# Optimization experiments

Measured on AMD Instinct MI355X. Metric: run time of the kernel, lower is better.

## Reference

```python
import jax, jax.numpy as jnp
import numpy as np

B, C, H, G, NCLS = 32, 256, 128, 128, 2  # graphs, nodes-per-graph==in_channels, hidden, matrix pool, classes
N = B * C                                # total nodes = 8192
E = 131072


def setup_inputs() -> dict:
    key = jax.random.key(0)
    ks = jax.random.split(key, 12)
    gain = 5.0 / 3.0
    xav = gain * np.sqrt(6.0 / (C + C))  # xavier_uniform bound for [C,C]
    return {
        "x": jax.random.normal(ks[0], (N, C), jnp.float32),
        "edge_index": jax.random.randint(ks[1], (2, E), 0, N),
        "graph_id": jax.random.randint(ks[2], (B,), 0, G),
        "batch": jnp.arange(N) // C,
        "pert_W": jax.random.uniform(ks[3], (G, C, C), jnp.float32, -xav, xav),
        "pert_b": jax.random.uniform(ks[4], (G, C, C), jnp.float32, -xav, xav),
        "mask_W": jax.random.uniform(ks[5], (G, C, C), jnp.float32, -xav, xav),
        "gcn_w0": jax.random.normal(ks[6], (C, H), jnp.float32) / np.sqrt(C),
        "gcn_w1": jax.random.normal(ks[7], (H, H), jnp.float32) / np.sqrt(H),
        "gcn_w2": jax.random.normal(ks[8], (H, H), jnp.float32) / np.sqrt(H),
        "mlp_W": jax.random.normal(ks[9], (2 * H, NCLS), jnp.float32) / np.sqrt(2 * H),
        "mlp_b": jnp.zeros((NCLS,), jnp.float32),
    }


def _hard_where(s):
    # MyWhere: 0 if s <= 0.5 else 1
    return jnp.where(s <= 0.5, 0.0, 1.0).astype(s.dtype)


def _predictor(x, adj, batch, gcn_w0, gcn_w1, gcn_w2, mlp_W, mlp_b):
    # GCN encoder: h <- relu(A @ h @ W); readout = concat(mean-pool, max-pool); MLP+sigmoid
    h = x
    for W in (gcn_w0, gcn_w1, gcn_w2):
        h = jax.nn.relu(adj @ (h @ W))
    sums = jax.ops.segment_sum(h, batch, num_segments=B)
    cnt = jax.ops.segment_sum(jnp.ones((h.shape[0], 1), h.dtype), batch, num_segments=B)
    mean = sums / jnp.maximum(cnt, 1.0)
    mx = jax.ops.segment_max(h, batch, num_segments=B)
    pooled = jnp.concatenate([mean, mx], axis=-1)  # [B, 2H]
    return jax.nn.sigmoid(pooled @ mlp_W + mlp_b)


def reference(x, edge_index, graph_id, batch, pert_W, pert_b, mask_W,
              gcn_w0, gcn_w1, gcn_w2, mlp_W, mlp_b):
    # dense adjacency (duplicate edges sum, matching sparse_coo.to_dense)
    adj = jnp.zeros((N, N), jnp.float32).at[edge_index[0], edge_index[1]].add(1.0)
    P = pert_W[graph_id]    # [B, C, C] block-diag blocks
    bias = pert_b[graph_id]  # [B, C, C] block-diag bias blocks
    # block_diag(P) @ adj == per-block GEMM over row stripes
    PA = jnp.einsum('bij,bjn->bin', P, adj.reshape(B, C, N))  # [B, C, N]
    PA = PA.reshape(B, C, B, C).at[jnp.arange(B), :, jnp.arange(B), :].add(bias)
    PA = PA.reshape(N, N)
    pert_adj = _hard_where(jax.nn.sigmoid(PA))
    M = _hard_where(jax.nn.sigmoid(mask_W[graph_id].reshape(N, C)))
    x_masked = M * x
    pred = _predictor(x, adj, batch, gcn_w0, gcn_w1, gcn_w2, mlp_W, mlp_b)
    aug_pred = _predictor(x_masked, pert_adj, batch, gcn_w0, gcn_w1, gcn_w2, mlp_W, mlp_b)
    return (adj, pert_adj, M, pred, aug_pred, x_masked)
```

## Files before the change

### kernel.cpp

```cpp
#include <hip/hip_runtime.h>
#include <hip/hip_bf16.h>

#define NN 8192
#define CC 256
#define BBg 32
#define HH 128
#define EE 131072

typedef __attribute__((ext_vector_type(8))) short short8;
typedef __attribute__((ext_vector_type(4))) float f32x4;
typedef unsigned long long ull;

__device__ __forceinline__ float hard01(float v) {
    if (v >= 1e-6f) return 1.0f;
    if (v <= 0.0f) return 0.0f;
    float ef = (float)exp(-(double)v);
    float s = 1.0f / (1.0f + ef);
    return (s > 0.5f) ? 1.0f : 0.0f;
}

__device__ __forceinline__ unsigned short f2bf(float f) {
    unsigned u = __float_as_uint(f);
    u += 0x7FFFu + ((u >> 16) & 1u);
    return (unsigned short)(u >> 16);
}
__device__ __forceinline__ float bf2f(unsigned short b) {
    return __uint_as_float(((unsigned)b) << 16);
}

__global__ void k_hist_mask(const int* __restrict__ ei, int* __restrict__ rowcnt,
                            int* __restrict__ colcnt, unsigned char* __restrict__ coljs,
                            const float* __restrict__ maskW, const int* __restrict__ gid,
                            const float* __restrict__ x, float* __restrict__ Mo,
                            float* __restrict__ xm) {
    int blk = blockIdx.x, t = threadIdx.x;
    if (blk < 512) {
        int e = blk * 256 + t;
        int r = ei[e], c = ei[EE + e];
        atomicAdd(&rowcnt[r], 1);
        int idx = (r >> 8) * NN + c;
        int slot = atomicAdd(&colcnt[idx], 1);
        if (slot < 16) coljs[(size_t)idx * 16 + slot] = (unsigned char)(r & 255);
    } else {
        int i = (blk - 512) * 256 + t;
        int base = i * 4;
        int r = base >> 8;
        int c = base & 255;
        int g = gid[r >> 8];
        float4 mv = *(const float4*)(maskW + ((size_t)g << 16) + ((size_t)(r & 255) << 8) + c);
        float4 xv = *(const float4*)(x + ((size_t)r << 8) + c);
        float4 m, o;
        m.x = hard01(mv.x); m.y = hard01(mv.y); m.z = hard01(mv.z); m.w = hard01(mv.w);
        o.x = m.x * xv.x; o.y = m.y * xv.y; o.z = m.z * xv.z; o.w = m.w * xv.w;
        *(float4*)(Mo + ((size_t)r << 8) + c) = m;
        *(float4*)(xm + ((size_t)r << 8) + c) = o;
    }
}

__global__ void __launch_bounds__(256) k_scan_pertadj(
        const int* __restrict__ rowcnt, int* __restrict__ rowptr,
        int* __restrict__ rowfill,
        const float* __restrict__ pertW, const float* __restrict__ pertB,
        const int* __restrict__ gid, const int* __restrict__ colcnt,
        const unsigned char* __restrict__ coljs,
        float* __restrict__ padj, unsigned char* __restrict__ padjbits) {
    __shared__ float Pl[32][257];
    __shared__ int sums[256];
    int t = threadIdx.x;
    if (blockIdx.x == 0) {
        int base = t * 32;
        int loc[32];
        int s = 0;
        #pragma unroll
        for (int i = 0; i < 32; ++i) { loc[i] = s; s += rowcnt[base + i]; }
        sums[t] = s;
        __syncthreads();
        if (t == 0) {
            int a = 0;
            for (int i = 0; i < 256; ++i) { int v = sums[i]; sums[i] = a; a += v; }
            rowptr[NN] = a;
        }
        __syncthreads();
        int off = sums[t];
        #pragma unroll
        for (int i = 0; i < 32; ++i) {
            rowptr[base + i] = off + loc[i];
            rowfill[base + i] = off + loc[i];
        }
        return;
    }
    int bid = blockIdx.x - 1;
    int nc = bid & 3, rt = (bid >> 2) & 7, b = bid >> 5;
    int g = gid[b];
    const float* src = pertW + ((size_t)g << 16) + (size_t)rt * 32 * CC;
    #pragma unroll 4
    for (int i = 0; i < 32; ++i) Pl[i][t] = src[i * CC + t];
    __syncthreads();
    int ty = t >> 6, tx = t & 63;
    int ro = ty * 8;
    const float* bsrc = pertB + ((size_t)g << 16) + (size_t)(rt * 32 + ro) * CC;
    for (int it = 0; it < 4; ++it) {
        int n0 = nc * 2048 + it * 512 + tx * 8;
        float s[8][8];
        #pragma unroll
        for (int ii = 0; ii < 8; ++ii)
            #pragma unroll
            for (int cc = 0; cc < 8; ++cc) s[ii][cc] = 0.0f;
        #pragma unroll
        for (int half = 0; half < 2; ++half) {
            int n = n0 + half * 4;
            int cidx = b * NN + n;
            int4 cnt4 = *(const int4*)(colcnt + cidx);
            const uint4* jp = (const uint4*)(coljs + (size_t)cidx * 16);
            #pragma unroll
            for (int cc = 0; cc < 4; ++cc) {
                int cnt = (&cnt4.x)[cc];
                cnt = cnt > 16 ? 16 : cnt;
                if (cnt == 0) continue;
                uint4 jv = jp[cc];
                for (int q = 0; q < cnt; ++q) {
                    unsigned word = (q < 8) ? ((q < 4) ? jv.x : jv.y)
                                            : ((q < 12) ? jv.z : jv.w);
                    int j = (word >> ((q & 3) * 8)) & 255;
                    #pragma unroll
                    for (int ii = 0; ii < 8; ++ii) s[ii][half * 4 + cc] += Pl[ro + ii][j];
                }
            }
        }
        bool diag = ((n0 >> 8) == b);
        #pragma unroll
        for (int ii = 0; ii < 8; ++ii) {
            if (diag) {
                const float* bp = bsrc + (size_t)ii * CC + (n0 & 255);
                #pragma unroll
                for (int cc = 0; cc < 8; ++cc) s[ii][cc] += bp[cc];
            }
            float f[8];
            unsigned byte = 0;
            #pragma unroll
            for (int cc = 0; cc < 8; ++cc) {
                f[cc] = hard01(s[ii][cc]);
                if (f[cc] != 0.f) byte |= (1u << cc);
            }
            size_t ob = (size_t)(b * CC + rt * 32 + ro + ii) * NN + n0;
            float4 f0, f1;
            f0.x = f[0]; f0.y = f[1]; f0.z = f[2]; f0.w = f[3];
            f1.x = f[4]; f1.y = f[5]; f1.z = f[6]; f1.w = f[7];
            *(float4*)(padj + ob) = f0;
            *(float4*)(padj + ob + 4) = f1;
            size_t bb = (size_t)(b * CC + rt * 32 + ro + ii) * (NN / 8)
                        + nc * 256 + it * 64 + tx;
            padjbits[bb] = (unsigned char)byte;
        }
    }
}

__device__ __forceinline__ void gemm_dual_body(
        int mt, int t,
        const float* __restrict__ Ap, const float* __restrict__ Aa,
        const float* __restrict__ W, float* __restrict__ Zp,
        unsigned short* __restrict__ Zthi, unsigned short* __restrict__ Ztlo,
        int K, int relu, int aparts, int apstride,
        float (*Alp)[68], float (*Ala)[68], float (*Wl)[132]) {
    int ty = t >> 3, tx = t & 7;
    float accp[16], acca[16];
    #pragma unroll
    for (int u = 0; u < 16; ++u) { accp[u] = 0.0f; acca[u] = 0.0f; }
    for (int kc = 0; kc < K; kc += 64) {
        int row = t >> 3, q = t & 7;
        {
            const float* ap = Ap + (size_t)(mt * 32 + row) * K + kc + q * 8;
            float4 f0 = *(const float4*)ap;
            float4 f1 = *(const float4*)(ap + 4);
            if (relu) {
                f0.x = fmaxf(f0.x, 0.f); f0.y = fmaxf(f0.y, 0.f);
                f0.z = fmaxf(f0.z, 0.f); f0.w = fmaxf(f0.w, 0.f);
                f1.x = fmaxf(f1.x, 0.f); f1.y = fmaxf(f1.y, 0.f);
                f1.z = fmaxf(f1.z, 0.f); f1.w = fmaxf(f1.w, 0.f);
            }
            *(float4*)&Alp[row][q * 8] = f0;
            *(float4*)&Alp[row][q * 8 + 4] = f1;
        }
        {
            const float* ap = Aa + (size_t)(mt * 32 + row) * K + kc + q * 8;
            float4 f0 = *(const float4*)ap;
            float4 f1 = *(const float4*)(ap + 4);
            for (int p = 1; p < aparts; ++p) {
                float4 g0 = *(const float4*)(ap + (size_t)p * apstride);
                float4 g1 = *(const float4*)(ap + (size_t)p * apstride + 4);
                f0.x += g0.x; f0.y += g0.y; f0.z += g0.z; f0.w += g0.w;
                f1.x += g1.x; f1.y += g1.y; f1.z += g1.z; f1.w += g1.w;
            }
            if (relu) {
                f0.x = fmaxf(f0.x, 0.f); f0.y = fmaxf(f0.y, 0.f);
                f0.z = fmaxf(f0.z, 0.f); f0.w = fmaxf(f0.w, 0.f);
                f1.x = fmaxf(f1.x, 0.f); f1.y = fmaxf(f1.y, 0.f);
                f1.z = fmaxf(f1.z, 0.f); f1.w = fmaxf(f1.w, 0.f);
            }
            *(float4*)&Ala[row][q * 8] = f0;
            *(float4*)&Ala[row][q * 8 + 4] = f1;
        }
        {
            int wrow = t >> 2, wq = t & 3;
            const float* wp = W + (size_t)(kc + wrow) * HH + wq * 32;
            #pragma unroll
            for (int u = 0; u < 32; u += 4)
                *(float4*)&Wl[wrow][wq * 32 + u] = *(const float4*)(wp + u);
        }
        __syncthreads();
        #pragma unroll 2
        for (int kk = 0; kk < 64; ++kk) {
            float a = Alp[ty][kk];
            float b2 = Ala[ty][kk];
            #pragma unroll
            for (int u = 0; u < 16; u += 4) {
                float4 wv = *(const float4*)(&Wl[kk][tx * 16 + u]);
                accp[u + 0] += a * wv.x; accp[u + 1] += a * wv.y;
                accp[u + 2] += a * wv.z; accp[u + 3] += a * wv.w;
                acca[u + 0] += b2 * wv.x; acca[u + 1] += b2 * wv.y;
                acca[u + 2] += b2 * wv.z; acca[u + 3] += b2 * wv.w;
            }
        }
        __syncthreads();
    }
    {
        float* cp = Zp + (size_t)(mt * 32 + ty) * HH + tx * 16;
        #pragma unroll
        for (int u = 0; u < 16; u += 4) {
            float4 f;
            f.x = accp[u]; f.y = accp[u + 1]; f.z = accp[u + 2]; f.w = accp[u + 3];
            *(float4*)(cp + u) = f;
        }
    }
    {
        __syncthreads();
        float* Tl = &Wl[0][0];
        #pragma unroll
        for (int u = 0; u < 16; ++u) Tl[ty * 132 + tx * 16 + u] = acca[u];
        __syncthreads();
        int col = t >> 1, half = t & 1;
        unsigned short hu[16] __attribute__((aligned(16)));
        unsigned short lu[16] __attribute__((aligned(16)));
        #pragma unroll
        for (int rr = 0; rr < 16; ++rr) {
            float v = Tl[(half * 16 + rr) * 132 + col];
            unsigned short hb = f2bf(v);
            hu[rr] = hb;
            lu[rr] = f2bf(v - bf2f(hb));
        }
        size_t ob = (size_t)col * NN + mt * 32 + half * 16;
        *(uint4*)(Zthi + ob)     = *(const uint4*)&hu[0];
        *(uint4*)(Zthi + ob + 8) = *(const uint4*)&hu[8];
        *(uint4*)(Ztlo + ob)     = *(const uint4*)&lu[0];
        *(uint4*)(Ztlo + ob + 8) = *(const uint4*)&lu[8];
    }
}

__global__ void __launch_bounds__(256) k_gemm_fill(
        const float* __restrict__ Ap, const float* __restrict__ Aa,
        const float* __restrict__ W, float* __restrict__ Zp,
        unsigned short* __restrict__ Zthi, unsigned short* __restrict__ Ztlo,
        int K, int relu, int aparts, int apstride,
        const int* __restrict__ ei, int* __restrict__ rowfill,
        int* __restrict__ csrcol) {
    __shared__ float Alp[32][68];
    __shared__ float Ala[32][68];
    __shared__ float Wl[64][132];
    int blk = blockIdx.x, t = threadIdx.x;
    if (blk < 256) {
        gemm_dual_body(blk, t, Ap, Aa, W, Zp, Zthi, Ztlo, K, relu, aparts, apstride,
                       Alp, Ala, Wl);
    } else {
        int e = (blk - 256) * 256 + t;
        int r = ei[e], c = ei[EE + e];
        int pos = atomicAdd(&rowfill[r], 1);
        csrcol[pos] = c;
    }
}

__global__ void __launch_bounds__(256) k_gemm_dual(
        const float* __restrict__ Ap, const float* __restrict__ Aa,
        const float* __restrict__ W, float* __restrict__ Zp,
        unsigned short* __restrict__ Zthi, unsigned short* __restrict__ Ztlo,
        int K, int relu, int aparts, int apstride) {
    __shared__ float Alp[32][68];
    __shared__ float Ala[32][68];
    __shared__ float Wl[64][132];
    gemm_dual_body(blockIdx.x, threadIdx.x, Ap, Aa, W, Zp, Zthi, Ztlo,
                   K, relu, aparts, apstride, Alp, Ala, Wl);
}

__device__ __forceinline__ void mfma_body(
        int blk, int t,
        const unsigned char* __restrict__ padjbits,
        const unsigned short* __restrict__ Zthi,
        const unsigned short* __restrict__ Ztlo,
        float* __restrict__ Sp, unsigned short* BhBase, unsigned short* BlBase) {
    int mt = blk & 31;
    int ncol = (blk >> 5) & 1;
    int sk = blk >> 6;
    int w = t >> 6, lane = t & 63;
    int quad = lane >> 4, l15 = lane & 15;
    f32x4 acc[4][4];
    #pragma unroll
    for (int m = 0; m < 4; ++m)
        #pragma unroll
        for (int i = 0; i < 4; ++i) acc[m][i] = (f32x4){0.f, 0.f, 0.f, 0.f};
    int bn = t >> 2, sub = t & 3;
    int bq = sub & 1, hilo = sub >> 1;
    const unsigned short* zsrc = (hilo ? Ztlo : Zthi)
        + (size_t)(ncol * 64 + bn) * NN + sk * 1024 + bq * 16;
    unsigned short* wb = hilo ? BlBase : BhBase;
    int row0 = mt * 256 + w * 64 + l15;
    const unsigned* ab[4];
    #pragma unroll
    for (int m = 0; m < 4; ++m)
        ab[m] = (const unsigned*)(padjbits + (size_t)(row0 + m * 16) * (NN / 8)) + sk * 32;
    int ldsw = bn * 40 + bq * 16;
    int bmb = l15 * 40 + quad * 8;
    uint4 rv0, rv1;
    unsigned bits[4], nbits[4];
    rv0 = *(const uint4*)(zsrc + 0);
    rv1 = *(const uint4*)(zsrc + 8);
    #pragma unroll
    for (int m = 0; m < 4; ++m) bits[m] = ab[m][0];
    *(uint4*)(wb + ldsw + 0) = rv0;
    *(uint4*)(wb + ldsw + 8) = rv1;
    __syncthreads();
    for (int st = 0; st < 32; ++st) {
        int cur = st & 1;
        if (st < 31) {
            int k = (st + 1) * 32;
            rv0 = *(const uint4*)(zsrc + k);
            rv1 = *(const uint4*)(zsrc + k + 8);
            #pragma unroll
            for (int m = 0; m < 4; ++m) nbits[m] = ab[m][st + 1];
        }
        short8 a[4];
        #pragma unroll
        for (int m = 0; m < 4; ++m) {
            unsigned byte = (bits[m] >> (quad * 8)) & 0xFFu;
            #pragma unroll
            for (int j = 0; j < 8; ++j)
                a[m][j] = (byte & (1u << j)) ? (short)0x3F80 : (short)0;
        }
        const unsigned short* Bh = BhBase + cur * 2560;
        const unsigned short* Bl = BlBase + cur * 2560;
        #pragma unroll
        for (int nt = 0; nt < 4; ++nt) {
            short8 fh = *(const short8*)(Bh + nt * 16 * 40 + bmb);
            short8 fl = *(const short8*)(Bl + nt * 16 * 40 + bmb);
            #pragma unroll
            for (int m = 0; m < 4; ++m) {
                acc[m][nt] = __builtin_amdgcn_mfma_f32_16x16x32_bf16(a[m], fh, acc[m][nt], 0, 0, 0);
                acc[m][nt] = __builtin_amdgcn_mfma_f32_16x16x32_bf16(a[m], fl, acc[m][nt], 0, 0, 0);
            }
        }
        if (st < 31) {
            unsigned short* wn = wb + (1 - cur) * 2560;
            *(uint4*)(wn + ldsw + 0) = rv0;
            *(uint4*)(wn + ldsw + 8) = rv1;
            #pragma unroll
            for (int m = 0; m < 4; ++m) bits[m] = nbits[m];
        }
        __syncthreads();
    }
    int dc = l15, dr = quad * 4;
    float* base = Sp + (size_t)sk * NN * HH
                + (size_t)(mt * 256 + w * 64 + dr) * HH + ncol * 64;
    #pragma unroll
    for (int m = 0; m < 4; ++m)
        #pragma unroll
        for (int nt = 0; nt < 4; ++nt)
            #pragma unroll
            for (int r = 0; r < 4; ++r)
                base[(size_t)(m * 16 + r) * HH + nt * 16 + dc] = acc[m][nt][r];
}

__device__ __forceinline__ void adj_body(
        int row, int t, unsigned* cnt,
        const int* __restrict__ rowptr, const int* __restrict__ csrcol,
        float* __restrict__ adj) {
    uint4 z = {0u, 0u, 0u, 0u};
    #pragma unroll
    for (int i = 0; i < 4; ++i) *(uint4*)&cnt[(i * 256 + t) * 4] = z;
    __syncthreads();
    int start = rowptr[row], end = rowptr[row + 1];
    for (int e = start + t; e < end; e += 256) {
        int c = csrcol[e];
        atomicAdd(&cnt[c >> 1], 1u << ((c & 1) * 16));
    }
    __syncthreads();
    float* dst = adj + (size_t)row * NN;
    #pragma unroll
    for (int i = 0; i < 8; ++i) {
        int p = i * 1024 + t * 4;
        unsigned w0 = cnt[p >> 1], w1 = cnt[(p >> 1) + 1];
        float4 f;
        f.x = (float)(w0 & 0xFFFFu); f.y = (float)(w0 >> 16);
        f.z = (float)(w1 & 0xFFFFu); f.w = (float)(w1 >> 16);
        *(float4*)(dst + p) = f;
    }
}

__device__ __forceinline__ void spmm_body(
        int bp, int t,
        const int* __restrict__ rowptr, const int* __restrict__ csrcol,
        const float* __restrict__ Z, float* __restrict__ S) {
    int row = bp * 2 + (t >> 7);
    int col = t & 127;
    int start = rowptr[row], end = rowptr[row + 1];
    float s0 = 0.f, s1 = 0.f;
    int e = start;
    for (; e + 2 <= end; e += 2) {
        int c0 = csrcol[e], c1 = csrcol[e + 1];
        s0 += Z[(size_t)c0 * HH + col];
        s1 += Z[(size_t)c1 * HH + col];
    }
    if (e < end) s0 += Z[(size_t)csrcol[e] * HH + col];
    S[(size_t)row * HH + col] = s0 + s1;
}

#define MFB 1024
#define SPB (NN / 2)

__global__ void __launch_bounds__(256, 4) k_mfma_adj_spmm(
        const unsigned char* __restrict__ padjbits,
        const unsigned short* __restrict__ Zthi,
        const unsigned short* __restrict__ Ztlo,
        float* __restrict__ Sp,
        const int* __restrict__ rowptr, const int* __restrict__ csrcol,
        float* __restrict__ adj,
        const float* __restrict__ Z, float* __restrict__ S) {
    __shared__ __align__(16) char smem[20480];
    int blk = blockIdx.x, t = threadIdx.x;
    if (blk < MFB) {
        mfma_body(blk, t, padjbits, Zthi, Ztlo, Sp,
                  (unsigned short*)smem, (unsigned short*)(smem + 10240));
    } else if (blk < MFB + SPB) {
        spmm_body(blk - MFB, t, rowptr, csrcol, Z, S);
    } else {
        adj_body(blk - (MFB + SPB), t, (unsigned*)smem, rowptr, csrcol, adj);
    }
}

__global__ void __launch_bounds__(256, 4) k_mfma_spmm2(
        const unsigned char* __restrict__ padjbits,
        const unsigned short* __restrict__ Zthi,
        const unsigned short* __restrict__ Ztlo,
        float* __restrict__ Sp,
        const int* __restrict__ rowptr, const int* __restrict__ csrcol,
        const float* __restrict__ Z, float* __restrict__ S) {
    __shared__ __align__(16) char smem[20480];
    int blk = blockIdx.x, t = threadIdx.x;
    if (blk < MFB) {
        mfma_body(blk, t, padjbits, Zthi, Ztlo, Sp,
                  (unsigned short*)smem, (unsigned short*)(smem + 10240));
    } else {
        spmm_body(blk - MFB, t, rowptr, csrcol, Z, S);
    }
}

__global__ void __launch_bounds__(256) k_pool2(const float* __restrict__ S,
                                               const float* __restrict__ Sp,
                                               const float* __restrict__ mlpW,
                                               const float* __restrict__ mlpb,
                                               float* __restrict__ pred,
                                               float* __restrict__ augp,
                                               int apstride) {
    __shared__ float ps[256], pm[256], pl[256], r0[256], r1[256];
    int aug = blockIdx.x >> 5, g = blockIdx.x & 31, t = threadIdx.x;
    const float* Sb = aug ? Sp : S;
    int parts = aug ? 8 : 1;
    float* outp = aug ? augp : pred;
    int col = t & 127, half = t >> 7;
    const float* base = Sb + (size_t)(g * CC + half * 128) * HH + col;
    float sum = 0.f, mx = -3.0e38f;
    for (int rr = 0; rr < 128; ++rr) {
        float v = base[(size_t)rr * HH];
        for (int p = 1; p < parts; ++p) v += base[(size_t)p * apstride + (size_t)rr * HH];
        v = fmaxf(v, 0.f);
        sum += v;
        mx = fmaxf(mx, v);
    }
    ps[t] = sum; pm[t] = mx;
    __syncthreads();
    if (half == 0) {
        pl[col] = (ps[col] + ps[col + 128]) * (1.0f / 256.0f);
        pl[col + 128] = fmaxf(pm[col], pm[col + 128]);
    }
    __syncthreads();
    r0[t] = pl[t] * mlpW[t * 2 + 0];
    r1[t] = pl[t] * mlpW[t * 2 + 1];
    __syncthreads();
    for (int sft = 128; sft > 0; sft >>= 1) {
        if (t < sft) { r0[t] += r0[t + sft]; r1[t] += r1[t + sft]; }
        __syncthreads();
    }
    if (t == 0) {
        float l0 = r0[0] + mlpb[0];
        float l1 = r1[0] + mlpb[1];
        outp[g * 2 + 0] = 1.0f / (1.0f + expf(-l0));
        outp[g * 2 + 1] = 1.0f / (1.0f + expf(-l1));
    }
}

extern "C" void kernel_launch(void* const* d_in, const int* in_sizes, int n_in,
                              void* d_out, int out_size, void* d_ws, size_t ws_size,
                              hipStream_t stream) {
    (void)in_sizes; (void)n_in; (void)out_size; (void)ws_size;
    const float* x     = (const float*)d_in[0];
    const int*   ei    = (const int*)d_in[1];
    const int*   gid   = (const int*)d_in[2];
    const float* pertW = (const float*)d_in[4];
    const float* pertB = (const float*)d_in[5];
    const float* maskW = (const float*)d_in[6];
    const float* w0    = (const float*)d_in[7];
    const float* w1    = (const float*)d_in[8];
    const float* w2    = (const float*)d_in[9];
    const float* mlpW  = (const float*)d_in[10];
    const float* mlpb  = (const float*)d_in[11];

    float* out  = (float*)d_out;
    float* adj  = out;
    float* padj = out + (size_t)NN * NN;
    float* Mo   = out + 2 * (size_t)NN * NN;
    float* pred = Mo + (size_t)NN * CC;
    float* augp = pred + (size_t)BBg * 2;
    float* xm   = augp + (size_t)BBg * 2;

    char* ws = (char*)d_ws;
    int*            colcnt   = (int*)ws;
    int*            rowcnt   = (int*)(ws + (1 << 20));
    int*            rowptr   = (int*)(ws + (1 << 20) + (64 << 10));
    int*            rowfill  = (int*)(ws + (1 << 20) + (128 << 10));
    unsigned char*  coljs    = (unsigned char*)(ws + (2 << 20));
    int*            csrcol   = (int*)(ws + (6 << 20));
    float*          Z        = (float*)(ws + (7 << 20));
    float*          S        = (float*)(ws + (11 << 20));
    unsigned short* Zthi     = (unsigned short*)(ws + (15 << 20));
    unsigned short* Ztlo     = (unsigned short*)(ws + (17 << 20));
    float*          Sp       = (float*)(ws + (19 << 20));
    unsigned char*  padjbits = (unsigned char*)(ws + (51 << 20));
    const int PS = NN * HH;

    hipMemsetAsync(colcnt, 0, (1 << 20) + (32 << 10), stream);
    k_hist_mask<<<2560, 256, 0, stream>>>(ei, rowcnt, colcnt, coljs,
                                          maskW, gid, x, Mo, xm);
    k_scan_pertadj<<<1025, 256, 0, stream>>>(rowcnt, rowptr, rowfill,
                                             pertW, pertB, gid, colcnt, coljs,
                                             padj, padjbits);
    k_gemm_fill<<<768, 256, 0, stream>>>(x, xm, w0, Z, Zthi, Ztlo, 256, 0, 1, 0,
                                         ei, rowfill, csrcol);
    k_mfma_adj_spmm<<<MFB + SPB + NN, 256, 0, stream>>>(
        padjbits, Zthi, Ztlo, Sp, rowptr, csrcol, adj, Z, S);
    k_gemm_dual<<<256, 256, 0, stream>>>(S, Sp, w1, Z, Zthi, Ztlo, 128, 1, 8, PS);
    k_mfma_spmm2<<<MFB + SPB, 256, 0, stream>>>(
        padjbits, Zthi, Ztlo, Sp, rowptr, csrcol, Z, S);
    k_gemm_dual<<<256, 256, 0, stream>>>(S, Sp, w2, Z, Zthi, Ztlo, 128, 1, 8, PS);
    k_mfma_spmm2<<<MFB + SPB, 256, 0, stream>>>(
        padjbits, Zthi, Ztlo, Sp, rowptr, csrcol, Z, S);
    k_pool2<<<64, 256, 0, stream>>>(S, Sp, mlpW, mlpb, pred, augp, PS);
}
```

Baseline: 1.112 ms.

## Split fused MFMA/SpMM/adj kernels and remap MFMA block indexing

```diff
diff --git a/kernel.cpp b/kernel.cpp
--- a/kernel.cpp
+++ b/kernel.cpp
@@ -296,9 +296,9 @@
         const unsigned short* __restrict__ Zthi,
         const unsigned short* __restrict__ Ztlo,
         float* __restrict__ Sp, unsigned short* BhBase, unsigned short* BlBase) {
-    int mt = blk & 31;
-    int ncol = (blk >> 5) & 1;
-    int sk = blk >> 6;
+    int sk = blk & 7;
+    int ncol = (blk >> 3) & 1;
+    int mt = blk >> 4;
     int w = t >> 6, lane = t & 63;
     int quad = lane >> 4, l15 = lane & 15;
     f32x4 acc[4][4];
@@ -373,41 +373,62 @@
         #pragma unroll
         for (int nt = 0; nt < 4; ++nt)
             #pragma unroll
-            for (int r = 0; r < 4; ++r)
-                base[(size_t)(m * 16 + r) * HH + nt * 16 + dc] = acc[m][nt][r];
-}
-
-__device__ __forceinline__ void adj_body(
-        int row, int t, unsigned* cnt,
+            for (int rr = 0; rr < 4; ++rr)
+                base[(size_t)(m * 16 + rr) * HH + nt * 16 + dc] = acc[m][nt][rr];
+}
+
+#define MFB 512
+
+__global__ void __launch_bounds__(256) k_mfma_adj(
+        const unsigned char* __restrict__ padjbits,
+        const unsigned short* __restrict__ Zthi,
+        const unsigned short* __restrict__ Ztlo,
+        float* __restrict__ Sp,
         const int* __restrict__ rowptr, const int* __restrict__ csrcol,
         float* __restrict__ adj) {
-    uint4 z = {0u, 0u, 0u, 0u};
-    #pragma unroll
-    for (int i = 0; i < 4; ++i) *(uint4*)&cnt[(i * 256 + t) * 4] = z;
-    __syncthreads();
-    int start = rowptr[row], end = rowptr[row + 1];
-    for (int e = start + t; e < end; e += 256) {
-        int c = csrcol[e];
-        atomicAdd(&cnt[c >> 1], 1u << ((c & 1) * 16));
-    }
-    __syncthreads();
-    float* dst = adj + (size_t)row * NN;
-    #pragma unroll
-    for (int i = 0; i < 8; ++i) {
-        int p = i * 1024 + t * 4;
-        unsigned w0 = cnt[p >> 1], w1 = cnt[(p >> 1) + 1];
-        float4 f;
-        f.x = (float)(w0 & 0xFFFFu); f.y = (float)(w0 >> 16);
-        f.z = (float)(w1 & 0xFFFFu); f.w = (float)(w1 >> 16);
-        *(float4*)(dst + p) = f;
-    }
-}
-
-__device__ __forceinline__ void spmm_body(
-        int bp, int t,
-        const int* __restrict__ rowptr, const int* __restrict__ csrcol,
-        const float* __restrict__ Z, float* __restrict__ S) {
-    int row = bp * 2 + (t >> 7);
+    __shared__ __align__(16) char smem[32768];
+    int blk = blockIdx.x, t = threadIdx.x;
+    if (blk < MFB) {
+        mfma_body(blk, t, padjbits, Zthi, Ztlo, Sp,
+                  (unsigned short*)smem, (unsigned short*)(smem + 10240));
+    } else {
+        int* cnt = (int*)smem;
+        int row = blk - MFB;
+        int4 z = make_int4(0, 0, 0, 0);
+        #pragma unroll
+        for (int i = 0; i < 8; ++i) *(int4*)&cnt[(i * 256 + t) * 4] = z;
+        __syncthreads();
+        int start = rowptr[row], end = rowptr[row + 1];
+        for (int e = start + t; e < end; e += 256) atomicAdd(&cnt[csrcol[e]], 1);
+        __syncthreads();
+        float* dst = adj + (size_t)row * NN;
+        #pragma unroll
+        for (int i = 0; i < 8; ++i) {
+            int p = i * 1024 + t * 4;
+            float4 f;
+            f.x = (float)cnt[p + 0]; f.y = (float)cnt[p + 1];
+            f.z = (float)cnt[p + 2]; f.w = (float)cnt[p + 3];
+            *(float4*)(dst + p) = f;
+        }
+    }
+}
+
+__global__ void __launch_bounds__(256) k_mfma_spmm(
+        const unsigned char* __restrict__ padjbits,
+        const unsigned short* __restrict__ Zthi,
+        const unsigned short* __restrict__ Ztlo,
+        float* __restrict__ Sp) {
+    __shared__ __align__(16) char smem[20480];
+    mfma_body(blockIdx.x, threadIdx.x, padjbits, Zthi, Ztlo, Sp,
+              (unsigned short*)smem, (unsigned short*)(smem + 10240));
+}
+
+__global__ void k_spmm_gather(const int* __restrict__ rowptr,
+                              const int* __restrict__ csrcol,
+                              const float* __restrict__ Z,
+                              float* __restrict__ S) {
+    int t = threadIdx.x;
+    int row = blockIdx.x * 2 + (t >> 7);
     int col = t & 127;
     int start = rowptr[row], end = rowptr[row + 1];
     float s0 = 0.f, s1 = 0.f;
@@ -419,46 +440,6 @@
     }
     if (e < end) s0 += Z[(size_t)csrcol[e] * HH + col];
     S[(size_t)row * HH + col] = s0 + s1;
-}
-
-#define MFB 1024
-#define SPB (NN / 2)
-
-__global__ void __launch_bounds__(256, 4) k_mfma_adj_spmm(
-        const unsigned char* __restrict__ padjbits,
-        const unsigned short* __restrict__ Zthi,
-        const unsigned short* __restrict__ Ztlo,
-        float* __restrict__ Sp,
-        const int* __restrict__ rowptr, const int* __restrict__ csrcol,
-        float* __restrict__ adj,
-        const float* __restrict__ Z, float* __restrict__ S) {
-    __shared__ __align__(16) char smem[20480];
-    int blk = blockIdx.x, t = threadIdx.x;
-    if (blk < MFB) {
-        mfma_body(blk, t, padjbits, Zthi, Ztlo, Sp,
-                  (unsigned short*)smem, (unsigned short*)(smem + 10240));
-    } else if (blk < MFB + SPB) {
-        spmm_body(blk - MFB, t, rowptr, csrcol, Z, S);
-    } else {
-        adj_body(blk - (MFB + SPB), t, (unsigned*)smem, rowptr, csrcol, adj);
-    }
-}
-
-__global__ void __launch_bounds__(256, 4) k_mfma_spmm2(
-        const unsigned char* __restrict__ padjbits,
-        const unsigned short* __restrict__ Zthi,
-        const unsigned short* __restrict__ Ztlo,
-        float* __restrict__ Sp,
-        const int* __restrict__ rowptr, const int* __restrict__ csrcol,
-        const float* __restrict__ Z, float* __restrict__ S) {
-    __shared__ __align__(16) char smem[20480];
-    int blk = blockIdx.x, t = threadIdx.x;
-    if (blk < MFB) {
-        mfma_body(blk, t, padjbits, Zthi, Ztlo, Sp,
-                  (unsigned short*)smem, (unsigned short*)(smem + 10240));
-    } else {
-        spmm_body(blk - MFB, t, rowptr, csrcol, Z, S);
-    }
 }
 
 __global__ void __launch_bounds__(256) k_pool2(const float* __restrict__ S,
@@ -552,13 +533,14 @@
                                              padj, padjbits);
     k_gemm_fill<<<768, 256, 0, stream>>>(x, xm, w0, Z, Zthi, Ztlo, 256, 0, 1, 0,
                                          ei, rowfill, csrcol);
-    k_mfma_adj_spmm<<<MFB + SPB + NN, 256, 0, stream>>>(
-        padjbits, Zthi, Ztlo, Sp, rowptr, csrcol, adj, Z, S);
+    k_mfma_adj<<<MFB + NN, 256, 0, stream>>>(padjbits, Zthi, Ztlo, Sp,
+                                             rowptr, csrcol, adj);
+    k_spmm_gather<<<NN / 2, 256, 0, stream>>>(rowptr, csrcol, Z, S);
     k_gemm_dual<<<256, 256, 0, stream>>>(S, Sp, w1, Z, Zthi, Ztlo, 128, 1, 8, PS);
-    k_mfma_spmm2<<<MFB + SPB, 256, 0, stream>>>(
-        padjbits, Zthi, Ztlo, Sp, rowptr, csrcol, Z, S);
+    k_spmm_gather<<<NN / 2, 256, 0, stream>>>(rowptr, csrcol, Z, S);
+    k_mfma_spmm<<<MFB, 256, 0, stream>>>(padjbits, Zthi, Ztlo, Sp);
     k_gemm_dual<<<256, 256, 0, stream>>>(S, Sp, w2, Z, Zthi, Ztlo, 128, 1, 8, PS);
-    k_mfma_spmm2<<<MFB + SPB, 256, 0, stream>>>(
-        padjbits, Zthi, Ztlo, Sp, rowptr, csrcol, Z, S);
+    k_spmm_gather<<<NN / 2, 256, 0, stream>>>(rowptr, csrcol, Z, S);
+    k_mfma_spmm<<<MFB, 256, 0, stream>>>(padjbits, Zthi, Ztlo, Sp);
     k_pool2<<<64, 256, 0, stream>>>(S, Sp, mlpW, mlpb, pred, augp, PS);
 }
```

Result: faster. 976.4 us (-12.2%).
